# Kernel tuning notes

Hardware: AMD Instinct MI355X
Metric: run time of the kernel (lower is better)

## Reference

```python
import jax, jax.numpy as jnp
import numpy as np

D_MODEL = 1024
N_HEADS = 16
HEAD_DIM = D_MODEL // N_HEADS


def setup_inputs() -> dict:
    key = jax.random.key(0)
    ks = jax.random.split(key, 5)
    T, B = 2048, 2
    scale = 1.0 / np.sqrt(D_MODEL)
    x = jax.random.normal(ks[0], (T, B, D_MODEL), dtype=jnp.float32)
    W_qkv = jax.random.normal(ks[1], (D_MODEL, 3 * D_MODEL), dtype=jnp.float32) * scale
    b_qkv = jnp.zeros((3 * D_MODEL,), dtype=jnp.float32)
    W_out = jax.random.normal(ks[2], (D_MODEL, D_MODEL), dtype=jnp.float32) * scale
    b_out = jnp.zeros((D_MODEL,), dtype=jnp.float32)
    return {"x": x, "W_qkv": W_qkv, "b_qkv": b_qkv, "W_out": W_out, "b_out": b_out}


def reference(x, W_qkv, b_qkv, W_out, b_out):
    T, B, D = x.shape
    H, Dh = N_HEADS, HEAD_DIM
    qkv = x @ W_qkv + b_qkv  # [T, B, 3D]
    q, k, v = jnp.split(qkv, 3, axis=-1)
    # [T, B, D] -> [B, H, T, Dh]
    def to_heads(t):
        return t.reshape(T, B, H, Dh).transpose(1, 2, 0, 3)
    q, k, v = to_heads(q), to_heads(k), to_heads(v)
    scores = jnp.einsum("bhqd,bhkd->bhqk", q, k) / jnp.sqrt(jnp.float32(Dh))
    causal = jnp.tril(jnp.ones((T, T), dtype=bool))  # True where attention allowed
    scores = jnp.where(causal, scores, -jnp.inf)
    attn = jax.nn.softmax(scores, axis=-1)
    context = jnp.einsum("bhqk,bhkd->bhqd", attn, v)  # [B, H, T, Dh]
    context = context.transpose(2, 0, 1, 3).reshape(T, B, D)  # [T, B, D]
    return context @ W_out + b_out
```

## Files before the change

kernel.cpp:

```cpp
#include <hip/hip_runtime.h>
#include <stdint.h>

#define T_SEQ 2048
#define BATCH 2
#define DMODEL 1024
#define NH 16
#define DH 64
#define M_ROWS (T_SEQ * BATCH)
#define N_QKV (3 * DMODEL)
#define BHQ (32 * T_SEQ)

typedef unsigned short u16;
using bf16x8 = __attribute__((ext_vector_type(8))) __bf16;
using f32x4  = __attribute__((ext_vector_type(4))) float;

__device__ __forceinline__ u16 f2bf(float f) {
    union { float f; uint32_t u; } v; v.f = f;
    uint32_t r = v.u + 0x7fffu + ((v.u >> 16) & 1u);
    return (u16)(r >> 16);
}

__device__ __forceinline__ uint32_t pack2(float a, float b) {
    union { float f; uint32_t u; } x, y; x.f = a; y.f = b;
    return (x.u >> 16) | (y.u & 0xffff0000u);
}

__device__ __forceinline__ float bf2f(u16 u) {
    union { uint32_t u; float f; } v; v.u = (uint32_t)u << 16;
    return v.f;
}

__device__ __forceinline__ void lds_load16(void* lds, const void* g) {
    auto lp = (__attribute__((address_space(3))) uint32_t*)(uint32_t)(uintptr_t)lds;
    auto gp = (const __attribute__((address_space(1))) uint32_t*)(uintptr_t)g;
    __builtin_amdgcn_global_load_lds(gp, lp, 16, 0, 0);
}

#define SCQ 0.18033688011112f


__global__ void cvt4_kernel(const float* __restrict__ in, u16* __restrict__ out, int n4) {
    int i = blockIdx.x * 256 + threadIdx.x;
    if (i < n4) {
        float4 v = ((const float4*)in)[i];
        union { u16 u[4]; uint2 d; } o;
        o.u[0] = f2bf(v.x); o.u[1] = f2bf(v.y); o.u[2] = f2bf(v.z); o.u[3] = f2bf(v.w);
        ((uint2*)out)[i] = o.d;
    }
}

__global__ void cvt_t_kernel(const float* __restrict__ in, u16* __restrict__ out, int R, int C) {
    __shared__ float t[32][33];
    int bx = blockIdx.x * 32;
    int by = blockIdx.y * 32;
    int tx = threadIdx.x & 31, ty = threadIdx.x >> 5;
#pragma unroll
    for (int rr = 0; rr < 32; rr += 8)
        t[ty + rr][tx] = in[(size_t)(by + ty + rr) * C + bx + tx];
    __syncthreads();
#pragma unroll
    for (int rr = 0; rr < 32; rr += 8)
        out[(size_t)(bx + ty + rr) * R + by + tx] = f2bf(t[tx][ty + rr]);
}


template<int EPI>
__global__ __launch_bounds__(256) void gemm_kernel(
    const u16* __restrict__ A, const u16* __restrict__ Bt,
    const float* __restrict__ bias,
    u16* __restrict__ outQ, u16* __restrict__ outK, u16* __restrict__ outV,
    float* __restrict__ outF,
    int M, int N, int K)
{
    __shared__ __align__(16) u16 lA[128 * 32];
    __shared__ __align__(16) u16 lB[128 * 32];

    const int tid  = threadIdx.x;
    const int bm   = blockIdx.y * 128;
    const int bn   = blockIdx.x * 128;
    const int lane = tid & 63;
    const int wid  = tid >> 6;
    const int wm   = (wid >> 1) * 64;
    const int wn   = (wid & 1) * 64;
    const int qr   = lane & 15;
    const int quad = lane >> 4;
    const int r4   = lane >> 2;
    const int c4   = (((lane & 3) ^ ((r4 >> 1) & 3))) * 8;
    const int sw   = (qr >> 1) & 3;

    f32x4 acc[4][4];
#pragma unroll
    for (int i = 0; i < 4; i++)
#pragma unroll
        for (int j = 0; j < 4; j++) acc[i][j] = f32x4{0.f, 0.f, 0.f, 0.f};

    for (int k0 = 0; k0 < K; k0 += 32) {
        __syncthreads();
#pragma unroll
        for (int cc = 0; cc < 2; cc++) {
            int c = wid + cc * 4;
            lds_load16(&lA[c * 512], &A [(size_t)(bm + 16 * c + r4) * K + k0 + c4]);
            lds_load16(&lB[c * 512], &Bt[(size_t)(bn + 16 * c + r4) * K + k0 + c4]);
        }
        __syncthreads();

        bf16x8 af[4], bfr[4];
#pragma unroll
        for (int i = 0; i < 4; i++)
            af[i] = *(const bf16x8*)&lA[(wm + i * 16 + qr) * 32 + ((quad ^ sw) * 8)];
#pragma unroll
        for (int j = 0; j < 4; j++)
            bfr[j] = *(const bf16x8*)&lB[(wn + j * 16 + qr) * 32 + ((quad ^ sw) * 8)];
#pragma unroll
        for (int i = 0; i < 4; i++)
#pragma unroll
            for (int j = 0; j < 4; j++)
                acc[i][j] = __builtin_amdgcn_mfma_f32_16x16x32_bf16(af[i], bfr[j], acc[i][j], 0, 0, 0);
    }

#pragma unroll
    for (int i = 0; i < 4; i++) {
#pragma unroll
        for (int j = 0; j < 4; j++) {
            int col = bn + wn + j * 16 + qr;
            float bv = bias[col];
#pragma unroll
            for (int r = 0; r < 4; r++) {
                int row = bm + wm + i * 16 + quad * 4 + r;
                float val = acc[i][j][r] + bv;
                if (EPI == 0) {
                    int t = row >> 1, b = row & 1;
                    int which = col >> 10;
                    int dm = col & 1023;
                    int h = dm >> 6, dh = dm & 63;
                    int bh = b * NH + h;
                    if (which == 0) {
                        outQ[((size_t)bh * T_SEQ + t) * DH + dh] = f2bf(val * SCQ);
                    } else if (which == 1) {
                        outK[((size_t)bh * T_SEQ + t) * DH + dh] = f2bf(val);
                    } else {
                        outV[((size_t)bh * DH + dh) * T_SEQ + t] = f2bf(val);
                    }
                } else {
                    outF[(size_t)row * N + col] = val;
                }
            }
        }
    }
}


__global__ __launch_bounds__(256) void attn_kernel(
    const u16* __restrict__ Qb, const u16* __restrict__ Kb,
    const u16* __restrict__ Vt,
    u16* __restrict__ Op, float* __restrict__ Lp)
{
    __shared__ __align__(16) u16 lK[64 * 64];
    __shared__ __align__(16) u16 lV[80 * 64];
    __shared__ __align__(16) u16 lP[4][32 * 64];

    const int bh   = blockIdx.x;
    const int qt   = 15 - blockIdx.y;
    const int seg  = blockIdx.z;
    const int tid  = threadIdx.x;
    const int lane = tid & 63;
    const int wid  = tid >> 6;
    const int qr   = lane & 15;
    const int quad = lane >> 4;
    const int sw   = qr & 7;

    const int srow = wid * 8 + (lane >> 3);
    const int scol = (((lane & 7) ^ ((lane >> 3) & 7))) * 8;

    {
        uint2 ones; ones.x = 0x3F803F80u; ones.y = 0x3F803F80u;
        *(uint2*)&lV[64 * 64 + tid * 4] = ones;
    }

    const u16* Q  = Qb + (size_t)bh * T_SEQ * DH;
    const u16* Kp = Kb + (size_t)bh * T_SEQ * DH;
    const u16* Vp = Vt + (size_t)bh * DH * T_SEQ;

    const int q0 = qt * 128 + wid * 32;

    bf16x8 qf[2][2];
#pragma unroll
    for (int g = 0; g < 2; g++)
#pragma unroll
        for (int ks = 0; ks < 2; ks++)
            qf[g][ks] = *(const bf16x8*)&Q[(size_t)(q0 + g * 16 + qr) * DH + ks * 32 + quad * 8];

    f32x4 o[2][5];
#pragma unroll
    for (int g = 0; g < 2; g++)
#pragma unroll
        for (int f = 0; f < 5; f++) o[g][f] = f32x4{0.f, 0.f, 0.f, 0.f};

    const int kt0 = seg * (qt + 1);
    const int kt1 = kt0 + (qt + 1);

    for (int kt = kt0; kt < kt1; kt++) {
        __syncthreads();
#pragma unroll
        for (int half = 0; half < 2; half++) {
            lds_load16(&lK[half * 2048 + wid * 512],
                       &Kp[(size_t)(kt * 64 + half * 32 + srow) * DH + scol]);
            lds_load16(&lV[half * 2048 + wid * 512],
                       &Vp[(size_t)(half * 32 + srow) * T_SEQ + kt * 64 + scol]);
        }
        __syncthreads();

        if (kt * 64 > q0 + 31) continue;

        f32x4 s[2][4];
#pragma unroll
        for (int g = 0; g < 2; g++)
#pragma unroll
            for (int fn = 0; fn < 4; fn++) s[g][fn] = f32x4{0.f, 0.f, 0.f, 0.f};
#pragma unroll
        for (int fn = 0; fn < 4; fn++)
#pragma unroll
            for (int ks = 0; ks < 2; ks++) {
                bf16x8 kf = *(const bf16x8*)&lK[(fn * 16 + qr) * 64 + (((ks * 4 + quad) ^ sw) * 8)];
#pragma unroll
                for (int g = 0; g < 2; g++)
                    s[g][fn] = __builtin_amdgcn_mfma_f32_16x16x32_bf16(kf, qf[g][ks], s[g][fn], 0, 0, 0);
            }

        if (kt * 64 + 63 > q0) {
#pragma unroll
            for (int g = 0; g < 2; g++) {
                int q = q0 + g * 16 + qr;
#pragma unroll
                for (int fn = 0; fn < 4; fn++) {
                    int key = kt * 64 + fn * 16 + quad * 4;
#pragma unroll
                    for (int r = 0; r < 4; r++)
                        if (key + r > q) s[g][fn][r] = -1e30f;
                }
            }
        }

#pragma unroll
        for (int g = 0; g < 2; g++) {
#pragma unroll
            for (int fn = 0; fn < 4; fn++) {
                float p0 = exp2f(s[g][fn][0]);
                float p1 = exp2f(s[g][fn][1]);
                float p2 = exp2f(s[g][fn][2]);
                float p3 = exp2f(s[g][fn][3]);
                uint2 w; w.x = pack2(p0, p1); w.y = pack2(p2, p3);
                int phys = ((fn * 2 + (quad >> 1)) ^ sw);
                *(uint2*)&lP[wid][(g * 16 + qr) * 64 + phys * 8 + (quad & 1) * 4] = w;
            }
        }

        bf16x8 pf[2][2];
#pragma unroll
        for (int g = 0; g < 2; g++)
#pragma unroll
            for (int ks = 0; ks < 2; ks++)
                pf[g][ks] = *(const bf16x8*)&lP[wid][(g * 16 + qr) * 64 + (((ks * 4 + quad) ^ sw) * 8)];
#pragma unroll
        for (int f = 0; f < 5; f++)
#pragma unroll
            for (int ks = 0; ks < 2; ks++) {
                bf16x8 vf = *(const bf16x8*)&lV[(f * 16 + qr) * 64 + (((ks * 4 + quad) ^ sw) * 8)];
#pragma unroll
                for (int g = 0; g < 2; g++)
                    o[g][f] = __builtin_amdgcn_mfma_f32_16x16x32_bf16(vf, pf[g][ks], o[g][f], 0, 0, 0);
            }
    }

#pragma unroll
    for (int g = 0; g < 2; g++) {
        int q = q0 + g * 16 + qr;
        size_t rbase = (size_t)seg * BHQ + (size_t)bh * T_SEQ + q;
        if (quad == 0) Lp[rbase] = o[g][4][0];
#pragma unroll
        for (int f = 0; f < 4; f++) {
            uint2 w;
            w.x = (uint32_t)f2bf(o[g][f][0]) | ((uint32_t)f2bf(o[g][f][1]) << 16);
            w.y = (uint32_t)f2bf(o[g][f][2]) | ((uint32_t)f2bf(o[g][f][3]) << 16);
            *(uint2*)&Op[rbase * 64 + f * 16 + quad * 4] = w;
        }
    }
}


__global__ void merge_kernel(const u16* __restrict__ Op, const float* __restrict__ Lp,
                             u16* __restrict__ ctx)
{
    int idx = blockIdx.x * 256 + threadIdx.x;
    int fq  = idx & 15;
    int q   = (idx >> 4) & (T_SEQ - 1);
    int bh  = idx >> 15;
    int b = bh >> 4, h = bh & 15;
    size_t rbase = (size_t)bh * T_SEQ + q;

    float invl = 1.0f / (Lp[rbase] + Lp[rbase + BHQ]);
    union { uint2 d; u16 u[4]; } a, c, r;
    a.d = *(const uint2*)&Op[rbase * 64 + fq * 4];
    c.d = *(const uint2*)&Op[(rbase + BHQ) * 64 + fq * 4];
#pragma unroll
    for (int i = 0; i < 4; i++)
        r.u[i] = f2bf((bf2f(a.u[i]) + bf2f(c.u[i])) * invl);
    *(uint2*)&ctx[((size_t)q * BATCH + b) * DMODEL + h * DH + fq * 4] = r.d;
}


extern "C" void kernel_launch(void* const* d_in, const int* in_sizes, int n_in,
                              void* d_out, int out_size, void* d_ws, size_t ws_size,
                              hipStream_t stream) {
    const float* x     = (const float*)d_in[0];
    const float* W_qkv = (const float*)d_in[1];
    const float* b_qkv = (const float*)d_in[2];
    const float* W_out = (const float*)d_in[3];
    const float* b_out = (const float*)d_in[4];
    float* out = (float*)d_out;

    char* ws = (char*)d_ws;
    u16* xb     = (u16*)(ws + 0);
    u16* wqkv_t = (u16*)(ws + (8u  << 20));
    u16* wout_t = (u16*)(ws + (14u << 20));
    u16* Qb     = (u16*)(ws + (16u << 20));
    u16* Kb     = (u16*)(ws + (24u << 20));
    u16* Vt     = (u16*)(ws + (32u << 20));
    float* Lp   = (float*)(ws + (40u << 20));
    u16* ctx    = xb;
    u16* Op     = (u16*)d_out;

    cvt4_kernel <<<(M_ROWS * DMODEL / 4) / 256, 256, 0, stream>>>(x, xb, M_ROWS * DMODEL / 4);
    cvt_t_kernel<<<dim3(N_QKV / 32, DMODEL / 32), 256, 0, stream>>>(W_qkv, wqkv_t, DMODEL, N_QKV);
    cvt_t_kernel<<<dim3(DMODEL / 32, DMODEL / 32), 256, 0, stream>>>(W_out, wout_t, DMODEL, DMODEL);

    gemm_kernel<0><<<dim3(N_QKV / 128, M_ROWS / 128), 256, 0, stream>>>(
        xb, wqkv_t, b_qkv, Qb, Kb, Vt, nullptr, M_ROWS, N_QKV, DMODEL);

    attn_kernel<<<dim3(BATCH * NH, T_SEQ / 128, 2), 256, 0, stream>>>(
        Qb, Kb, Vt, Op, Lp);

    merge_kernel<<<(BHQ * 16) / 256, 256, 0, stream>>>(Op, Lp, ctx);

    gemm_kernel<1><<<dim3(DMODEL / 128, M_ROWS / 128), 256, 0, stream>>>(
        ctx, wout_t, b_out, nullptr, nullptr, nullptr, out, M_ROWS, DMODEL, DMODEL);
}
```

Baseline: 209.4 us.

## Double-buffer attention K/V tiles, merge weight transposes, narrow output GEMM tiles

The attention kernel now double-buffers K and V tiles in LDS, prefetching the next tile while the current one is computed and dropping one barrier per iteration. The row-sum ones tile becomes a register constant, and the P staging buffer shrinks to one 16-row group reused per g. The two weight-transpose launches are merged into one kernel, and the output projection GEMM uses 128x64 tiles so it launches twice as many blocks. The cost is more LDS for the K/V double buffer. The single barrier per iteration relies on the prefetch not overwriting the buffer other waves are still reading, and on the async loads completing before that barrier.

```diff
diff --git a/kernel.cpp b/kernel.cpp
--- a/kernel.cpp
+++ b/kernel.cpp
@@ -49,9 +49,13 @@
     }
 }
 
-__global__ void cvt_t_kernel(const float* __restrict__ in, u16* __restrict__ out, int R, int C) {
+__global__ void cvt_t2_kernel(const float* __restrict__ A, u16* __restrict__ oA,
+                              const float* __restrict__ B, u16* __restrict__ oB) {
     __shared__ float t[32][33];
-    int bx = blockIdx.x * 32;
+    const int R = 1024;
+    const float* in; u16* out; int C, bx;
+    if (blockIdx.x < 96) { in = A; out = oA; C = 3072; bx = blockIdx.x * 32; }
+    else                 { in = B; out = oB; C = 1024; bx = (blockIdx.x - 96) * 32; }
     int by = blockIdx.y * 32;
     int tx = threadIdx.x & 31, ty = threadIdx.x >> 5;
 #pragma unroll
@@ -64,7 +68,7 @@
 }
 
 
-template<int EPI>
+template<int EPI, int NF>
 __global__ __launch_bounds__(256) void gemm_kernel(
     const u16* __restrict__ A, const u16* __restrict__ Bt,
     const float* __restrict__ bias,
@@ -73,55 +77,57 @@
     int M, int N, int K)
 {
     __shared__ __align__(16) u16 lA[128 * 32];
-    __shared__ __align__(16) u16 lB[128 * 32];
+    __shared__ __align__(16) u16 lB[NF * 32 * 32];
 
     const int tid  = threadIdx.x;
     const int bm   = blockIdx.y * 128;
-    const int bn   = blockIdx.x * 128;
+    const int bn   = blockIdx.x * (NF * 32);
     const int lane = tid & 63;
     const int wid  = tid >> 6;
     const int wm   = (wid >> 1) * 64;
-    const int wn   = (wid & 1) * 64;
+    const int wn   = (wid & 1) * (NF * 16);
     const int qr   = lane & 15;
     const int quad = lane >> 4;
     const int r4   = lane >> 2;
     const int c4   = (((lane & 3) ^ ((r4 >> 1) & 3))) * 8;
     const int sw   = (qr >> 1) & 3;
 
-    f32x4 acc[4][4];
+    f32x4 acc[4][NF];
 #pragma unroll
     for (int i = 0; i < 4; i++)
 #pragma unroll
-        for (int j = 0; j < 4; j++) acc[i][j] = f32x4{0.f, 0.f, 0.f, 0.f};
+        for (int j = 0; j < NF; j++) acc[i][j] = f32x4{0.f, 0.f, 0.f, 0.f};
 
     for (int k0 = 0; k0 < K; k0 += 32) {
         __syncthreads();
 #pragma unroll
         for (int cc = 0; cc < 2; cc++) {
             int c = wid + cc * 4;
-            lds_load16(&lA[c * 512], &A [(size_t)(bm + 16 * c + r4) * K + k0 + c4]);
+            lds_load16(&lA[c * 512], &A[(size_t)(bm + 16 * c + r4) * K + k0 + c4]);
+        }
+#pragma unroll
+        for (int c = wid; c < 2 * NF; c += 4)
             lds_load16(&lB[c * 512], &Bt[(size_t)(bn + 16 * c + r4) * K + k0 + c4]);
-        }
         __syncthreads();
 
-        bf16x8 af[4], bfr[4];
+        bf16x8 af[4], bfr[NF];
 #pragma unroll
         for (int i = 0; i < 4; i++)
             af[i] = *(const bf16x8*)&lA[(wm + i * 16 + qr) * 32 + ((quad ^ sw) * 8)];
 #pragma unroll
-        for (int j = 0; j < 4; j++)
+        for (int j = 0; j < NF; j++)
             bfr[j] = *(const bf16x8*)&lB[(wn + j * 16 + qr) * 32 + ((quad ^ sw) * 8)];
 #pragma unroll
         for (int i = 0; i < 4; i++)
 #pragma unroll
-            for (int j = 0; j < 4; j++)
+            for (int j = 0; j < NF; j++)
                 acc[i][j] = __builtin_amdgcn_mfma_f32_16x16x32_bf16(af[i], bfr[j], acc[i][j], 0, 0, 0);
     }
 
 #pragma unroll
     for (int i = 0; i < 4; i++) {
 #pragma unroll
-        for (int j = 0; j < 4; j++) {
+        for (int j = 0; j < NF; j++) {
             int col = bn + wn + j * 16 + qr;
             float bv = bias[col];
 #pragma unroll
@@ -155,9 +161,9 @@
     const u16* __restrict__ Vt,
     u16* __restrict__ Op, float* __restrict__ Lp)
 {
-    __shared__ __align__(16) u16 lK[64 * 64];
-    __shared__ __align__(16) u16 lV[80 * 64];
-    __shared__ __align__(16) u16 lP[4][32 * 64];
+    __shared__ __align__(16) u16 lK[2][64 * 64];
+    __shared__ __align__(16) u16 lV[2][64 * 64];
+    __shared__ __align__(16) u16 lP[4][16 * 64];
 
     const int bh   = blockIdx.x;
     const int qt   = 15 - blockIdx.y;
@@ -172,11 +178,6 @@
     const int srow = wid * 8 + (lane >> 3);
     const int scol = (((lane & 7) ^ ((lane >> 3) & 7))) * 8;
 
-    {
-        uint2 ones; ones.x = 0x3F803F80u; ones.y = 0x3F803F80u;
-        *(uint2*)&lV[64 * 64 + tid * 4] = ones;
-    }
-
     const u16* Q  = Qb + (size_t)bh * T_SEQ * DH;
     const u16* Kp = Kb + (size_t)bh * T_SEQ * DH;
     const u16* Vp = Vt + (size_t)bh * DH * T_SEQ;
@@ -190,6 +191,10 @@
         for (int ks = 0; ks < 2; ks++)
             qf[g][ks] = *(const bf16x8*)&Q[(size_t)(q0 + g * 16 + qr) * DH + ks * 32 + quad * 8];
 
+    bf16x8 onesf;
+#pragma unroll
+    for (int j = 0; j < 8; j++) onesf[j] = (__bf16)1.0f;
+
     f32x4 o[2][5];
 #pragma unroll
     for (int g = 0; g < 2; g++)
@@ -199,17 +204,27 @@
     const int kt0 = seg * (qt + 1);
     const int kt1 = kt0 + (qt + 1);
 
-    for (int kt = kt0; kt < kt1; kt++) {
+#pragma unroll
+    for (int half = 0; half < 2; half++) {
+        lds_load16(&lK[0][half * 2048 + wid * 512],
+                   &Kp[(size_t)(kt0 * 64 + half * 32 + srow) * DH + scol]);
+        lds_load16(&lV[0][half * 2048 + wid * 512],
+                   &Vp[(size_t)(half * 32 + srow) * T_SEQ + kt0 * 64 + scol]);
+    }
+
+    int p = 0;
+    for (int kt = kt0; kt < kt1; kt++, p ^= 1) {
         __syncthreads();
-#pragma unroll
-        for (int half = 0; half < 2; half++) {
-            lds_load16(&lK[half * 2048 + wid * 512],
-                       &Kp[(size_t)(kt * 64 + half * 32 + srow) * DH + scol]);
-            lds_load16(&lV[half * 2048 + wid * 512],
-                       &Vp[(size_t)(half * 32 + srow) * T_SEQ + kt * 64 + scol]);
-        }
-        __syncthreads();
-
+        if (kt + 1 < kt1) {
+            int nb = p ^ 1;
+#pragma unroll
+            for (int half = 0; half < 2; half++) {
+                lds_load16(&lK[nb][half * 2048 + wid * 512],
+                           &Kp[(size_t)((kt + 1) * 64 + half * 32 + srow) * DH + scol]);
+                lds_load16(&lV[nb][half * 2048 + wid * 512],
+                           &Vp[(size_t)(half * 32 + srow) * T_SEQ + (kt + 1) * 64 + scol]);
+            }
+        }
         if (kt * 64 > q0 + 31) continue;
 
         f32x4 s[2][4];
@@ -221,7 +236,7 @@
         for (int fn = 0; fn < 4; fn++)
 #pragma unroll
             for (int ks = 0; ks < 2; ks++) {
-                bf16x8 kf = *(const bf16x8*)&lK[(fn * 16 + qr) * 64 + (((ks * 4 + quad) ^ sw) * 8)];
+                bf16x8 kf = *(const bf16x8*)&lK[p][(fn * 16 + qr) * 64 + (((ks * 4 + quad) ^ sw) * 8)];
 #pragma unroll
                 for (int g = 0; g < 2; g++)
                     s[g][fn] = __builtin_amdgcn_mfma_f32_16x16x32_bf16(kf, qf[g][ks], s[g][fn], 0, 0, 0);
@@ -241,6 +256,7 @@
             }
         }
 
+        bf16x8 pf[2][2];
 #pragma unroll
         for (int g = 0; g < 2; g++) {
 #pragma unroll
@@ -251,21 +267,19 @@
                 float p3 = exp2f(s[g][fn][3]);
                 uint2 w; w.x = pack2(p0, p1); w.y = pack2(p2, p3);
                 int phys = ((fn * 2 + (quad >> 1)) ^ sw);
-                *(uint2*)&lP[wid][(g * 16 + qr) * 64 + phys * 8 + (quad & 1) * 4] = w;
-            }
-        }
-
-        bf16x8 pf[2][2];
-#pragma unroll
-        for (int g = 0; g < 2; g++)
+                *(uint2*)&lP[wid][qr * 64 + phys * 8 + (quad & 1) * 4] = w;
+            }
 #pragma unroll
             for (int ks = 0; ks < 2; ks++)
-                pf[g][ks] = *(const bf16x8*)&lP[wid][(g * 16 + qr) * 64 + (((ks * 4 + quad) ^ sw) * 8)];
+                pf[g][ks] = *(const bf16x8*)&lP[wid][qr * 64 + (((ks * 4 + quad) ^ sw) * 8)];
+        }
+
 #pragma unroll
         for (int f = 0; f < 5; f++)
 #pragma unroll
             for (int ks = 0; ks < 2; ks++) {
-                bf16x8 vf = *(const bf16x8*)&lV[(f * 16 + qr) * 64 + (((ks * 4 + quad) ^ sw) * 8)];
+                bf16x8 vf = (f == 4) ? onesf
+                    : *(const bf16x8*)&lV[p][(f * 16 + qr) * 64 + (((ks * 4 + quad) ^ sw) * 8)];
 #pragma unroll
                 for (int g = 0; g < 2; g++)
                     o[g][f] = __builtin_amdgcn_mfma_f32_16x16x32_bf16(vf, pf[g][ks], o[g][f], 0, 0, 0);
@@ -330,11 +344,10 @@
     u16* ctx    = xb;
     u16* Op     = (u16*)d_out;
 
-    cvt4_kernel <<<(M_ROWS * DMODEL / 4) / 256, 256, 0, stream>>>(x, xb, M_ROWS * DMODEL / 4);
-    cvt_t_kernel<<<dim3(N_QKV / 32, DMODEL / 32), 256, 0, stream>>>(W_qkv, wqkv_t, DMODEL, N_QKV);
-    cvt_t_kernel<<<dim3(DMODEL / 32, DMODEL / 32), 256, 0, stream>>>(W_out, wout_t, DMODEL, DMODEL);
-
-    gemm_kernel<0><<<dim3(N_QKV / 128, M_ROWS / 128), 256, 0, stream>>>(
+    cvt4_kernel  <<<(M_ROWS * DMODEL / 4) / 256, 256, 0, stream>>>(x, xb, M_ROWS * DMODEL / 4);
+    cvt_t2_kernel<<<dim3(128, 32), 256, 0, stream>>>(W_qkv, wqkv_t, W_out, wout_t);
+
+    gemm_kernel<0, 4><<<dim3(N_QKV / 128, M_ROWS / 128), 256, 0, stream>>>(
         xb, wqkv_t, b_qkv, Qb, Kb, Vt, nullptr, M_ROWS, N_QKV, DMODEL);
 
     attn_kernel<<<dim3(BATCH * NH, T_SEQ / 128, 2), 256, 0, stream>>>(
@@ -342,6 +355,6 @@
 
     merge_kernel<<<(BHQ * 16) / 256, 256, 0, stream>>>(Op, Lp, ctx);
 
-    gemm_kernel<1><<<dim3(DMODEL / 128, M_ROWS / 128), 256, 0, stream>>>(
+    gemm_kernel<1, 2><<<dim3(DMODEL / 64, M_ROWS / 128), 256, 0, stream>>>(
         ctx, wout_t, b_out, nullptr, nullptr, nullptr, out, M_ROWS, DMODEL, DMODEL);
 }
```

Result: faster. 194.8 us (-7.0%).
